# Kernel tuning notes

Hardware: AMD Instinct MI355X
Metric: run time of the kernel (lower is better)

## Reference

```python
import jax, jax.numpy as jnp
import numpy as np

DIM = 1024
FACTOR = 32          # factor_size
SUB = 8              # sub_blocks = (dim // factor_size) // 4
RANK = 8
B, T = 48, 256


def hamilton(A_stack):
    # A_stack: (rank, 4, SUB, SUB) -> H: (rank, 4*SUB, 4*SUB)
    r, i, j, k = A_stack[:, 0], A_stack[:, 1], A_stack[:, 2], A_stack[:, 3]
    row0 = jnp.concatenate([r, -i, -j, -k], axis=2)
    row1 = jnp.concatenate([i,  r, -k,  j], axis=2)
    row2 = jnp.concatenate([j,  k,  r, -i], axis=2)
    row3 = jnp.concatenate([k, -j,  i,  r], axis=2)
    return jnp.concatenate([row0, row1, row2, row3], axis=1)


def setup_inputs() -> dict:
    key = jax.random.key(0)
    k1, k2, k3 = jax.random.split(key, 3)
    x = jax.random.normal(k1, (B, T, DIM), dtype=jnp.float32)
    A_stack = jax.random.normal(k2, (RANK, 4, SUB, SUB), dtype=jnp.float32)
    # factors_B: orthogonal-init then scaled by (rank_index)^-0.5; random normal
    # scaled similarly is numerically equivalent in structure for the reference.
    scales = (jnp.arange(1, RANK + 1, dtype=jnp.float32) ** -0.5)[:, None, None]
    B_stack = jax.random.normal(k3, (RANK, FACTOR, FACTOR), dtype=jnp.float32) * scales
    bias = jnp.zeros((DIM,), dtype=jnp.float32)
    return {"x": x, "A_stack": A_stack, "B_stack": B_stack, "bias": bias}


def reference(x, A_stack, B_stack, bias):
    Bb, Tt, D = x.shape
    x_flat = x.reshape(-1, 4 * SUB, FACTOR)           # (n, 32, 32)
    H = hamilton(A_stack)                              # (r, 32, 32)
    wave_mod = jnp.einsum('nsi,rji->rnsj', x_flat, B_stack)   # (r, n, 32, 32)
    wave_out = jnp.einsum('rnsj,rks->nkj', wave_mod, H)       # (n, 32, 32)
    return wave_out.reshape(Bb, Tt, D) + bias
```

## Files before the change

kernel.cpp:

```cpp
#include <hip/hip_runtime.h>
#include <hip/hip_bf16.h>
#include <stdint.h>

#define M_TOT 12288
#define K_DIM 1024
#define N_DIM 1024
#define NTILE 16

#define LDSBUF 57344

typedef __attribute__((ext_vector_type(8))) __bf16 bf16x8;
typedef __attribute__((ext_vector_type(4))) float  f32x4;

__global__ __launch_bounds__(256)
void make_w(const float* __restrict__ A4,
            const float* __restrict__ Bs,
            __bf16* __restrict__ W)
{
    int idx = blockIdx.x * 256 + threadIdx.x;
    int dout = idx >> 10;
    int din  = idx & 1023;
    int k = dout >> 5, j = dout & 31;
    int s = din  >> 5, i = din  & 31;
    int kb = k >> 3, k8 = k & 7;
    int sb = s >> 3, s8 = s & 7;

    const int   comp[4][4] = {{0,1,2,3},{1,0,3,2},{2,3,0,1},{3,2,1,0}};
    const float sgn [4][4] = {{1.f,-1.f,-1.f,-1.f},
                              {1.f, 1.f,-1.f, 1.f},
                              {1.f, 1.f, 1.f,-1.f},
                              {1.f,-1.f, 1.f, 1.f}};
    int   c  = comp[kb][sb];
    float sg = sgn [kb][sb];

    float acc = 0.f;
    #pragma unroll
    for (int r = 0; r < 8; ++r) {
        float h = A4[((r*4 + c)*8 + k8)*8 + s8];
        float b = Bs[(r*32 + j)*32 + i];
        acc += h * b;
    }
    W[idx] = (__bf16)(sg * acc);
}

__global__ __launch_bounds__(256)
void cvt_x(const float* __restrict__ X, __bf16* __restrict__ Xb)
{
    size_t t = (size_t)blockIdx.x * 256 + threadIdx.x;
    const float4* x4 = (const float4*)X;
    float4 a = x4[2*t + 0];
    float4 b = x4[2*t + 1];
    bf16x8 v;
    v[0] = (__bf16)a.x; v[1] = (__bf16)a.y; v[2] = (__bf16)a.z; v[3] = (__bf16)a.w;
    v[4] = (__bf16)b.x; v[5] = (__bf16)b.y; v[6] = (__bf16)b.z; v[7] = (__bf16)b.w;
    *(bf16x8*)&Xb[t * 8] = v;
}

__device__ __forceinline__ void gl_lds16(const void* g, void* l)
{
    __builtin_amdgcn_global_load_lds(
        (const __attribute__((address_space(1))) void*)g,
        (__attribute__((address_space(3))) void*)l,
        16, 0, 0);
}

#define PHASE_MFMA(SUB, NH, BF)                                                 \
    __builtin_amdgcn_s_barrier();                                               \
    asm volatile("s_waitcnt lgkmcnt(0)" ::: "memory");                          \
    __builtin_amdgcn_sched_barrier(0);                                          \
    __builtin_amdgcn_s_setprio(1);                                              \
    _Pragma("unroll")                                                           \
    for (int mi = 0; mi < 3; ++mi) {                                            \
        _Pragma("unroll")                                                       \
        for (int ni = 0; ni < 2; ++ni) {                                        \
            acc[(SUB)*3+mi][(NH)*2+ni] = __builtin_amdgcn_mfma_f32_16x16x32_bf16(\
                aF[mi][0], BF[ni][0], acc[(SUB)*3+mi][(NH)*2+ni], 0, 0, 0);     \
            acc[(SUB)*3+mi][(NH)*2+ni] = __builtin_amdgcn_mfma_f32_16x16x32_bf16(\
                aF[mi][1], BF[ni][1], acc[(SUB)*3+mi][(NH)*2+ni], 0, 0, 0);     \
        }                                                                       \
    }                                                                           \
    __builtin_amdgcn_s_setprio(0);                                              \
    __builtin_amdgcn_s_barrier();

__global__ __launch_bounds__(512, 2)
void gemm8p(const __bf16* __restrict__ A,
            const __bf16* __restrict__ BT,
            const float*  __restrict__ bias,
            float* __restrict__ C)
{
    __shared__ __align__(16) char lds[2 * LDSBUF];

    const int tid  = threadIdx.x;
    const int wave = tid >> 6;
    const int lane = tid & 63;

    int wg  = blockIdx.x;
    int swz = (wg & 7) * 32 + (wg >> 3);
    const int brow = (swz >> 2) * 192;
    const int bcol = (swz & 3)  * 256;

    const int mg = wave >> 2;
    const int ng = wave & 3;
    const int fr = lane & 15;
    const int kq = lane >> 4;

    f32x4 acc[6][4];
    #pragma unroll
    for (int i = 0; i < 6; ++i)
        #pragma unroll
        for (int j = 0; j < 4; ++j)
            acc[i][j] = (f32x4){0.f, 0.f, 0.f, 0.f};

    auto stageA = [&](int ta) {
        if (ta >= NTILE) return;
        char* region = lds + (ta & 1) * LDSBUF;
        #pragma unroll
        for (int q = 0; q < 3; ++q) {
            int s    = q * 8192 + tid * 16;
            int rwh  = s >> 7;
            int colb = (s & 127) ^ ((rwh & 7) << 4);
            const char* src = (const char*)A +
                ((size_t)(brow + rwh) * K_DIM + ta * 64) * 2 + colb;
            gl_lds16(src, region + q * 8192 + wave * 1024);
        }
    };
    auto stageB = [&](int ta, int nh) {
        if (ta >= NTILE) return;
        char* region = lds + (ta & 1) * LDSBUF + 24576 + nh * 16384;
        #pragma unroll
        for (int q = 0; q < 2; ++q) {
            int s    = q * 8192 + tid * 16;
            int rwh  = s >> 7;
            int colb = (s & 127) ^ ((rwh & 7) << 4);
            int absr = ((rwh >> 5) << 6) + nh * 32 + (rwh & 31);
            const char* src = (const char*)BT +
                ((size_t)(bcol + absr) * K_DIM + ta * 64) * 2 + colb;
            gl_lds16(src, region + q * 8192 + wave * 1024);
        }
    };

    bf16x8 aF[3][2], bF0[2][2], bF1[2][2];

    auto ldA = [&](int bufb, int sub) {
        const char* base = lds + bufb;
        #pragma unroll
        for (int mi = 0; mi < 3; ++mi) {
            int rwh = mg * 96 + sub * 48 + mi * 16 + fr;
            #pragma unroll
            for (int ks = 0; ks < 2; ++ks) {
                int col = (ks * 64 + kq * 16) ^ ((rwh & 7) << 4);
                aF[mi][ks] = *(const bf16x8*)(base + rwh * 128 + col);
            }
        }
    };
    auto ldB = [&](bf16x8 (&bF)[2][2], int bufb, int nh) {
        const char* base = lds + bufb + 24576 + nh * 16384;
        #pragma unroll
        for (int ni = 0; ni < 2; ++ni) {
            int rwh = ng * 32 + ni * 16 + fr;
            #pragma unroll
            for (int ks = 0; ks < 2; ++ks) {
                int col = (ks * 64 + kq * 16) ^ ((rwh & 7) << 4);
                bF[ni][ks] = *(const bf16x8*)(base + rwh * 128 + col);
            }
        }
    };

    stageA(0); stageB(0, 0); stageB(0, 1);
    stageA(1);
    asm volatile("s_waitcnt vmcnt(3)" ::: "memory");
    __builtin_amdgcn_s_barrier();

    for (int t = 0; t < NTILE; ++t) {
        const int bufb = (t & 1) * LDSBUF;

        ldA(bufb, 0);
        ldB(bF0, bufb, 0);
        stageB(t + 1, 0);
        PHASE_MFMA(0, 0, bF0)

        ldB(bF1, bufb, 1);
        stageB(t + 1, 1);
        PHASE_MFMA(0, 1, bF1)

        ldA(bufb, 1);
        PHASE_MFMA(1, 1, bF1)

        stageA(t + 2);
        __builtin_amdgcn_s_barrier();
        __builtin_amdgcn_s_setprio(1);
        #pragma unroll
        for (int mi = 0; mi < 3; ++mi) {
            #pragma unroll
            for (int ni = 0; ni < 2; ++ni) {
                acc[3+mi][ni] = __builtin_amdgcn_mfma_f32_16x16x32_bf16(
                    aF[mi][0], bF0[ni][0], acc[3+mi][ni], 0, 0, 0);
                acc[3+mi][ni] = __builtin_amdgcn_mfma_f32_16x16x32_bf16(
                    aF[mi][1], bF0[ni][1], acc[3+mi][ni], 0, 0, 0);
            }
        }
        __builtin_amdgcn_s_setprio(0);
        if (t < NTILE - 2) {
            asm volatile("s_waitcnt vmcnt(3)" ::: "memory");
        } else {
            asm volatile("s_waitcnt vmcnt(0)" ::: "memory");
        }
        __builtin_amdgcn_s_barrier();
    }

    #pragma unroll
    for (int mf = 0; mf < 6; ++mf) {
        int r0 = brow + mg * 96 + mf * 16 + kq * 4;
        #pragma unroll
        for (int nf = 0; nf < 4; ++nf) {
            int c0 = bcol + ng * 64 + nf * 16 + fr;
            float bv = bias[c0];
            #pragma unroll
            for (int j = 0; j < 4; ++j)
                C[(size_t)(r0 + j) * N_DIM + c0] = acc[mf][nf][j] + bv;
        }
    }
}

extern "C" void kernel_launch(void* const* d_in, const int* in_sizes, int n_in,
                              void* d_out, int out_size, void* d_ws, size_t ws_size,
                              hipStream_t stream)
{
    const float* x    = (const float*)d_in[0];
    const float* A4   = (const float*)d_in[1];
    const float* Bs   = (const float*)d_in[2];
    const float* bias = (const float*)d_in[3];
    float* out = (float*)d_out;

    __bf16* W  = (__bf16*)d_ws;
    __bf16* Xb = (__bf16*)((char*)d_ws + (size_t)(1<<21));

    make_w<<<4096, 256, 0, stream>>>(A4, Bs, W);
    cvt_x<<<(M_TOT * K_DIM / 8 + 255) / 256, 256, 0, stream>>>(x, Xb);

    gemm8p<<<256, 512, 0, stream>>>(Xb, W, bias, out);
}
```

Measured before the change: 129.7 us.

## Fuse fp32-to-bf16 conversion of X into GEMM A-tile loading

Removes the separate cvt_x kernel. The GEMM now loads fp32 X tiles into registers one tile ahead, converts them to bf16, and writes them swizzled into LDS, replacing the direct global-to-LDS bf16 loads. This avoids writing and re-reading a 24 MB bf16 copy of X and saves one kernel launch. In exchange it adds register pressure, since 6 float4 values are held per thread, and VALU conversion work inside the main loop, and it changes the vmcnt wait accounting.

```diff
diff --git a/kernel.cpp b/kernel.cpp
--- a/kernel.cpp
+++ b/kernel.cpp
@@ -10,6 +10,7 @@
 #define LDSBUF 57344
 
 typedef __attribute__((ext_vector_type(8))) __bf16 bf16x8;
+typedef __attribute__((ext_vector_type(4))) __bf16 bf16x4;
 typedef __attribute__((ext_vector_type(4))) float  f32x4;
 
 __global__ __launch_bounds__(256)
@@ -41,19 +42,6 @@
         acc += h * b;
     }
     W[idx] = (__bf16)(sg * acc);
-}
-
-__global__ __launch_bounds__(256)
-void cvt_x(const float* __restrict__ X, __bf16* __restrict__ Xb)
-{
-    size_t t = (size_t)blockIdx.x * 256 + threadIdx.x;
-    const float4* x4 = (const float4*)X;
-    float4 a = x4[2*t + 0];
-    float4 b = x4[2*t + 1];
-    bf16x8 v;
-    v[0] = (__bf16)a.x; v[1] = (__bf16)a.y; v[2] = (__bf16)a.z; v[3] = (__bf16)a.w;
-    v[4] = (__bf16)b.x; v[5] = (__bf16)b.y; v[6] = (__bf16)b.z; v[7] = (__bf16)b.w;
-    *(bf16x8*)&Xb[t * 8] = v;
 }
 
 __device__ __forceinline__ void gl_lds16(const void* g, void* l)
@@ -83,7 +71,7 @@
     __builtin_amdgcn_s_barrier();
 
 __global__ __launch_bounds__(512, 2)
-void gemm8p(const __bf16* __restrict__ A,
+void gemm8p(const float* __restrict__ X,
             const __bf16* __restrict__ BT,
             const float*  __restrict__ bias,
             float* __restrict__ C)
@@ -111,17 +99,38 @@
         for (int j = 0; j < 4; ++j)
             acc[i][j] = (f32x4){0.f, 0.f, 0.f, 0.f};
 
-    auto stageA = [&](int ta) {
+    float4 aPre[3][2];
+
+    auto loadA = [&](int ta) {
+        if (ta >= NTILE) return;
+        #pragma unroll
+        for (int c = 0; c < 3; ++c) {
+            #pragma unroll
+            for (int p = 0; p < 2; ++p) {
+                int s   = c * 16384 + p * 8192 + tid * 16;
+                int row = s >> 8;
+                const float* src = X + (size_t)(brow + row) * K_DIM
+                                     + ta * 64 + ((s & 255) >> 2);
+                aPre[c][p] = *(const float4*)src;
+            }
+        }
+    };
+    auto writeA = [&](int ta) {
         if (ta >= NTILE) return;
         char* region = lds + (ta & 1) * LDSBUF;
         #pragma unroll
-        for (int q = 0; q < 3; ++q) {
-            int s    = q * 8192 + tid * 16;
-            int rwh  = s >> 7;
-            int colb = (s & 127) ^ ((rwh & 7) << 4);
-            const char* src = (const char*)A +
-                ((size_t)(brow + rwh) * K_DIM + ta * 64) * 2 + colb;
-            gl_lds16(src, region + q * 8192 + wave * 1024);
+        for (int c = 0; c < 3; ++c) {
+            #pragma unroll
+            for (int p = 0; p < 2; ++p) {
+                int sb   = c * 8192 + p * 4096 + tid * 8;
+                int row  = sb >> 7;
+                int colb = (sb & 127) ^ ((row & 7) << 4);
+                float4 f = aPre[c][p];
+                bf16x4 v;
+                v[0] = (__bf16)f.x; v[1] = (__bf16)f.y;
+                v[2] = (__bf16)f.z; v[3] = (__bf16)f.w;
+                *(bf16x4*)(region + row * 128 + colb) = v;
+            }
         }
     };
     auto stageB = [&](int ta, int nh) {
@@ -166,9 +175,12 @@
         }
     };
 
-    stageA(0); stageB(0, 0); stageB(0, 1);
-    stageA(1);
-    asm volatile("s_waitcnt vmcnt(3)" ::: "memory");
+    loadA(0);
+    stageB(0, 0); stageB(0, 1);
+    asm volatile("s_waitcnt vmcnt(4)" ::: "memory");
+    writeA(0);
+    loadA(1);
+    asm volatile("s_waitcnt vmcnt(6) lgkmcnt(0)" ::: "memory");
     __builtin_amdgcn_s_barrier();
 
     for (int t = 0; t < NTILE; ++t) {
@@ -186,7 +198,11 @@
         ldA(bufb, 1);
         PHASE_MFMA(1, 1, bF1)
 
-        stageA(t + 2);
+        if (t + 1 < NTILE) {
+            asm volatile("s_waitcnt vmcnt(4)" ::: "memory");
+            writeA(t + 1);
+            loadA(t + 2);
+        }
         __builtin_amdgcn_s_barrier();
         __builtin_amdgcn_s_setprio(1);
         #pragma unroll
@@ -201,9 +217,9 @@
         }
         __builtin_amdgcn_s_setprio(0);
         if (t < NTILE - 2) {
-            asm volatile("s_waitcnt vmcnt(3)" ::: "memory");
+            asm volatile("s_waitcnt vmcnt(6) lgkmcnt(0)" ::: "memory");
         } else {
-            asm volatile("s_waitcnt vmcnt(0)" ::: "memory");
+            asm volatile("s_waitcnt vmcnt(0) lgkmcnt(0)" ::: "memory");
         }
         __builtin_amdgcn_s_barrier();
     }
@@ -232,11 +248,8 @@
     const float* bias = (const float*)d_in[3];
     float* out = (float*)d_out;
 
-    __bf16* W  = (__bf16*)d_ws;
-    __bf16* Xb = (__bf16*)((char*)d_ws + (size_t)(1<<21));
+    __bf16* W = (__bf16*)d_ws;
 
     make_w<<<4096, 256, 0, stream>>>(A4, Bs, W);
-    cvt_x<<<(M_TOT * K_DIM / 8 + 255) / 256, 256, 0, stream>>>(x, Xb);
-
-    gemm8p<<<256, 512, 0, stream>>>(Xb, W, bias, out);
-}
+    gemm8p<<<256, 512, 0, stream>>>(x, W, bias, out);
+}
```

New measurement: 132.4 us. 1.02x slower.
